# Optimization experiments

Hardware: AMD Instinct MI355X
Metric: run time of the kernel (lower is better)

Reference implementation:

```python
import jax, jax.numpy as jnp
import numpy as np

N = 4096        # nodes
C = 256         # in_channels
E0 = 65536      # edges before adding self-loops
RATIO = 0.5
K = int(np.ceil(RATIO * N))   # pooled nodes (topk)
NEG = 0.2       # leaky relu negative slope


def setup_inputs() -> dict:
    key = jax.random.key(0)
    ks = jax.random.split(key, 12)
    x = jax.random.normal(ks[0], (N, C), jnp.float32)
    src = jax.random.randint(ks[1], (E0,), 0, N)
    off = jax.random.randint(ks[2], (E0,), 1, N)
    dst = (src + off) % N                      # guaranteed no self-loops
    edge_index = jnp.stack([src, dst]).astype(jnp.int32)
    s = 1.0 / np.sqrt(C)
    s2 = 1.0 / np.sqrt(2 * C)
    u = lambda k, shape, b: jax.random.uniform(k, shape, jnp.float32, -b, b)
    return dict(
        x=x, edge_index=edge_index,
        Wq=u(ks[3], (C, C), s), bq=u(ks[4], (C,), s),          # lin_q
        gat_w=u(ks[5], (2 * C,), s2), gat_b=u(ks[6], (1,), s2),  # gat_att
        le1_w=u(ks[7], (C,), s), le1_b=u(ks[8], (1,), s),      # LEConv lin1
        le2_w=u(ks[9], (C,), s),                                # LEConv lin2 (no bias)
        le3_w=u(ks[10], (C,), s), le3_b=u(ks[11], (1,), s),    # LEConv lin3
    )


def _asap(x, edge_index, Wq, bq, gat_w, gat_b, le1_w, le1_b, le2_w, le3_w, le3_b):
    # add_remaining_self_loops (inputs have none -> all N loops, weight 1)
    loops = jnp.arange(N, dtype=edge_index.dtype)
    ei = jnp.concatenate([edge_index, jnp.stack([loops, loops])], axis=1)
    i, j = ei[0], ei[1]          # i: aggregation target, j: neighbor

    x_pool = x                   # GNN is None -> x_pool = x
    xj = x_pool[j]               # [E, C]

    # Master2Token attention: X_q = scatter_max over target i
    Xq = jax.ops.segment_max(xj, i, num_segments=N)       # [N, C]
    Mq = Xq @ Wq + bq                                     # lin_q
    sc = jnp.concatenate([Mq[i], xj], axis=-1) @ gat_w + gat_b[0]  # [E]
    sc = jnp.where(sc > 0, sc, NEG * sc)                  # leaky relu

    # segment softmax over targets i
    m = jax.ops.segment_max(sc, i, num_segments=N)
    e = jnp.exp(sc - m[i])
    z = jax.ops.segment_sum(e, i, num_segments=N)
    score = e / z[i]                                      # dropout_att=0, eval

    # cluster representation
    out = jax.ops.segment_sum(x[j] * score[:, None], i, num_segments=N)  # [N, C]

    # fitness = sigmoid(LEConv(out)): x_i' = lin3(x_i) + sum_j (lin1(x_j) - lin2(x_i))
    a = out @ le1_w + le1_b[0]                            # [N]
    b = out @ le2_w                                       # [N]
    agg = jax.ops.segment_sum(a[j] - b[i], i, num_segments=N)
    fitness = jax.nn.sigmoid(agg + out @ le3_w + le3_b[0])  # [N]

    # topk pooling (single graph -> global top_k)
    fit_k, perm = jax.lax.top_k(fitness, K)
    x_out = out[perm] * fit_k[:, None]                    # [K, C]

    # graph_connectivity: E = S^T A S (dense stand-in for coalesce+spspmm)
    n_idx = jnp.zeros(N, jnp.int32).at[perm].set(jnp.arange(K, dtype=jnp.int32))
    in_perm = jnp.zeros(N, bool).at[perm].set(True)
    sS = jax.lax.stop_gradient(score) * in_perm[i]        # score.detach(), kept-cluster edges
    S = jnp.zeros((N, K), x.dtype).at[j, n_idx[i]].add(sS)   # S[j, new(i)] = score
    A = jnp.zeros((N, N), x.dtype).at[i, j].add(1.0)      # edge_weight None -> ones, coalesced
    Eadj = S.T @ (A @ S)                                  # [K, K]
    # remove_self_loops then add_remaining_self_loops(fill=1)
    Eadj = Eadj - jnp.diag(jnp.diag(Eadj)) + jnp.eye(K, dtype=Eadj.dtype)
    return x_out, Eadj, perm


def reference(x, edge_index, Wq, bq, gat_w, gat_b, le1_w, le1_b, le2_w, le3_w, le3_b):
    return _asap(x, edge_index, Wq, bq, gat_w, gat_b,
                 le1_w, le1_b, le2_w, le3_w, le3_b)
```

## Files before the change

### kernel.cpp

```cpp
#include <hip/hip_runtime.h>
#include <math.h>

constexpr int NN  = 4096;
constexpr int CC  = 256;
constexpr int EE0 = 65536;
constexpr int EE  = 69632;
constexpr int KK  = 2048;
constexpr int SL  = 128;

__device__ __forceinline__ void edge_ij(const int* __restrict__ ei, int e, int& i, int& j) {
    if (e < EE0) { i = ei[e]; j = ei[EE0 + e]; }
    else         { i = e - EE0; j = i; }
}
__device__ __forceinline__ int edge_i(const int* __restrict__ ei, int e) {
    return (e < EE0) ? ei[e] : e - EE0;
}
__device__ __forceinline__ int edge_j(const int* __restrict__ ei, int e) {
    return (e < EE0) ? ei[EE0 + e] : e - EE0;
}

__global__ __launch_bounds__(256) void k_build(const int* __restrict__ ei,
                                               int* cnt_i, int* cnt_j,
                                               int* lst_i, int* lst_j,
                                               const float* __restrict__ Wq, const float* __restrict__ bq,
                                               const float* __restrict__ gat_w, const float* __restrict__ gat_b,
                                               double* wv, double* consts, int EB) {
    if ((int)blockIdx.x < EB) {
        int e = blockIdx.x * 256 + threadIdx.x;
        if (e >= EE) return;
        int i, j; edge_ij(ei, e, i, j);
        int si = atomicAdd(&cnt_i[i], 1);
        lst_i[i * SL + si] = e;
        int sj = atomicAdd(&cnt_j[j], 1);
        lst_j[j * SL + sj] = e;
        return;
    }
    int k = blockIdx.x - EB, c = threadIdx.x, l = c & 63;
    double s = (double)Wq[k * CC + c] * (double)gat_w[c];
    #pragma unroll
    for (int d = 32; d > 0; d >>= 1) s += __shfl_down(s, d, 64);
    __shared__ double red[4];
    if (l == 0) red[c >> 6] = s;
    __syncthreads();
    if (c == 0) wv[k] = red[0] + red[1] + red[2] + red[3];
    if (k == 0 && c == 0) {
        double cb = 0.0;
        for (int q = 0; q < CC; ++q) cb += (double)bq[q] * (double)gat_w[q];
        consts[0] = cb + (double)gat_b[0];
    }
}

__global__ __launch_bounds__(256) void k_attn(const float* __restrict__ x, const int* __restrict__ ei,
                                              const int* __restrict__ cnt_i, const int* __restrict__ lst_i,
                                              const double* __restrict__ wv, const float* __restrict__ gat_w,
                                              const double* __restrict__ consts,
                                              const float* __restrict__ le1_w, const float* __restrict__ le1_b,
                                              const float* __restrict__ le2_w,
                                              const float* __restrict__ le3_w, const float* __restrict__ le3_b,
                                              float* __restrict__ score32, float* __restrict__ out32,
                                              double* a64, double* b64, double* l3v) {
    __shared__ int    sj[SL];
    __shared__ double ssc[SL];
    __shared__ double mz[2];
    __shared__ union { float4 m4[4][64]; double d[4][CC]; } red;

    const int n = blockIdx.x, t = threadIdx.x, g = t >> 6, l = t & 63;
    const int base = n * SL;
    const int deg = cnt_i[n];
    const float* gw2 = gat_w + CC;

    float4 mx = make_float4(-INFINITY, -INFINITY, -INFINITY, -INFINITY);
    for (int p = g; p < deg; p += 4) {
        int e = lst_i[base + p];
        int j = edge_j(ei, e);
        float4 v = ((const float4*)(x + (size_t)j * CC))[l];
        mx.x = fmaxf(mx.x, v.x); mx.y = fmaxf(mx.y, v.y);
        mx.z = fmaxf(mx.z, v.z); mx.w = fmaxf(mx.w, v.w);
        double d = (double)v.x * (double)gw2[4 * l]     + (double)v.y * (double)gw2[4 * l + 1]
                 + (double)v.z * (double)gw2[4 * l + 2] + (double)v.w * (double)gw2[4 * l + 3];
        #pragma unroll
        for (int dd = 32; dd > 0; dd >>= 1) d += __shfl_down(d, dd, 64);
        if (l == 0) { sj[p] = j; ssc[p] = d; }
    }
    red.m4[g][l] = mx;
    __syncthreads();
    if (g == 0) {
        float4 a = red.m4[0][l], b = red.m4[1][l], c2 = red.m4[2][l], d4 = red.m4[3][l];
        float m0 = fmaxf(fmaxf(a.x, b.x), fmaxf(c2.x, d4.x));
        float m1 = fmaxf(fmaxf(a.y, b.y), fmaxf(c2.y, d4.y));
        float m2 = fmaxf(fmaxf(a.z, b.z), fmaxf(c2.z, d4.z));
        float m3 = fmaxf(fmaxf(a.w, b.w), fmaxf(c2.w, d4.w));
        double alph = (double)m0 * wv[4 * l]     + (double)m1 * wv[4 * l + 1]
                    + (double)m2 * wv[4 * l + 2] + (double)m3 * wv[4 * l + 3];
        #pragma unroll
        for (int dd = 32; dd > 0; dd >>= 1) alph += __shfl_down(alph, dd, 64);
        if (l == 0) mz[0] = alph + consts[0];
    }
    __syncthreads();
    double an = mz[0];
    for (int p = t; p < deg; p += 256) {
        double v = an + ssc[p];
        ssc[p] = v > 0.0 ? v : 0.2 * v;
    }
    __syncthreads();
    if (t < 64) {
        double mm = -1e300;
        for (int p = l; p < deg; p += 64) mm = fmax(mm, ssc[p]);
        #pragma unroll
        for (int d = 32; d > 0; d >>= 1) mm = fmax(mm, __shfl_xor(mm, d, 64));
        double z = 0.0;
        for (int p = l; p < deg; p += 64) z += exp(ssc[p] - mm);
        #pragma unroll
        for (int d = 32; d > 0; d >>= 1) z += __shfl_xor(z, d, 64);
        if (l == 0) { mz[0] = mm; mz[1] = 1.0 / z; }
    }
    __syncthreads();
    double mm = mz[0], inv = mz[1];
    for (int p = t; p < deg; p += 256) {
        double sc = exp(ssc[p] - mm) * inv;
        ssc[p] = sc;
        score32[lst_i[base + p]] = (float)sc;
    }
    __syncthreads();
    double a0 = 0, a1 = 0, a2 = 0, a3 = 0;
    for (int p = g; p < deg; p += 4) {
        double sc = ssc[p];
        float4 v = ((const float4*)(x + (size_t)sj[p] * CC))[l];
        a0 += sc * (double)v.x; a1 += sc * (double)v.y;
        a2 += sc * (double)v.z; a3 += sc * (double)v.w;
    }
    red.d[g][4 * l + 0] = a0; red.d[g][4 * l + 1] = a1;
    red.d[g][4 * l + 2] = a2; red.d[g][4 * l + 3] = a3;
    __syncthreads();
    if (g == 0) {
        double o0 = red.d[0][4*l]   + red.d[1][4*l]   + red.d[2][4*l]   + red.d[3][4*l];
        double o1 = red.d[0][4*l+1] + red.d[1][4*l+1] + red.d[2][4*l+1] + red.d[3][4*l+1];
        double o2 = red.d[0][4*l+2] + red.d[1][4*l+2] + red.d[2][4*l+2] + red.d[3][4*l+2];
        double o3 = red.d[0][4*l+3] + red.d[1][4*l+3] + red.d[2][4*l+3] + red.d[3][4*l+3];
        float4 ov; ov.x = (float)o0; ov.y = (float)o1; ov.z = (float)o2; ov.w = (float)o3;
        ((float4*)(out32 + (size_t)n * CC))[l] = ov;
        float4 w1 = ((const float4*)le1_w)[l];
        float4 w2 = ((const float4*)le2_w)[l];
        float4 w3 = ((const float4*)le3_w)[l];
        double s1 = o0 * (double)w1.x + o1 * (double)w1.y + o2 * (double)w1.z + o3 * (double)w1.w;
        double s2 = o0 * (double)w2.x + o1 * (double)w2.y + o2 * (double)w2.z + o3 * (double)w2.w;
        double s3 = o0 * (double)w3.x + o1 * (double)w3.y + o2 * (double)w3.z + o3 * (double)w3.w;
        #pragma unroll
        for (int dd = 32; dd > 0; dd >>= 1) {
            s1 += __shfl_down(s1, dd, 64);
            s2 += __shfl_down(s2, dd, 64);
            s3 += __shfl_down(s3, dd, 64);
        }
        if (l == 0) {
            a64[n] = s1 + (double)le1_b[0];
            b64[n] = s2;
            l3v[n] = s3 + (double)le3_b[0];
        }
    }
}

__global__ __launch_bounds__(256) void k_zlog(const int* __restrict__ ei,
                                              const int* __restrict__ cnt_i, const int* __restrict__ lst_i,
                                              const double* __restrict__ a64, const double* __restrict__ b64,
                                              const double* __restrict__ l3v, double* zlog) {
    int n = blockIdx.x * 4 + (threadIdx.x >> 6);
    int l = threadIdx.x & 63;
    int deg = cnt_i[n];
    int base = n * SL;
    double acc = 0.0;
    for (int p = l; p < deg; p += 64) {
        int e = lst_i[base + p];
        acc += a64[edge_j(ei, e)];
    }
    #pragma unroll
    for (int d = 32; d > 0; d >>= 1) acc += __shfl_xor(acc, d, 64);
    if (l == 0) zlog[n] = acc - (double)deg * b64[n] + l3v[n];
}

__global__ __launch_bounds__(256) void k_rank(const double* __restrict__ zlog,
                                              const float* __restrict__ out32,
                                              int* __restrict__ perm, int* __restrict__ n_idx,
                                              float* __restrict__ xout, float* __restrict__ operm) {
    int n = blockIdx.x, t = threadIdx.x;
    double zn = zlog[n];
    int cnt = 0;
    #pragma unroll
    for (int u = 0; u < NN / 256; ++u) {
        int m = t + u * 256;
        double zm = zlog[m];
        cnt += ((zm > zn) || (zm == zn && m < n)) ? 1 : 0;
    }
    #pragma unroll
    for (int d = 32; d > 0; d >>= 1) cnt += __shfl_down(cnt, d, 64);
    __shared__ int red[4];
    __shared__ int rr;
    if ((t & 63) == 0) red[t >> 6] = cnt;
    __syncthreads();
    if (t == 0) {
        int r = red[0] + red[1] + red[2] + red[3];
        rr = r;
        if (r < KK) {
            perm[r] = n;
            n_idx[n] = r;
            operm[r] = (float)n;
        } else {
            n_idx[n] = -1;
        }
    }
    __syncthreads();
    int r = rr;
    if (r < KK) {
        double fit = 1.0 / (1.0 + exp(-zn));
        xout[(size_t)r * CC + t] = (float)((double)out32[(size_t)n * CC + t] * fit);
    }
}

__global__ __launch_bounds__(256) void k_colval(const int* __restrict__ ei,
                                                const int* __restrict__ cnt_j, const int* __restrict__ lst_j,
                                                const int* __restrict__ n_idx, const float* __restrict__ score32,
                                                int* __restrict__ colj, float* __restrict__ svalj) {
    int p = blockIdx.x * 256 + threadIdx.x;
    int n = p >> 7, s = p & (SL - 1);
    if (s >= cnt_j[n]) return;
    int e = lst_j[p];
    colj[p] = n_idx[edge_i(ei, e)];
    svalj[p] = score32[e];
}

__global__ __launch_bounds__(256) void k_eadj(const int* __restrict__ ei,
                                              const int* __restrict__ cnt_i, const int* __restrict__ lst_i,
                                              const int* __restrict__ cnt_j,
                                              const int* __restrict__ perm,
                                              const float* __restrict__ score32,
                                              const int* __restrict__ colj, const float* __restrict__ svalj,
                                              float* __restrict__ Ead) {
    __shared__ float row[KK];
    int r = blockIdx.x, t = threadIdx.x;
    float4 z4 = make_float4(0.f, 0.f, 0.f, 0.f);
    for (int c = t; c < KK / 4; c += 256) ((float4*)row)[c] = z4;
    __syncthreads();
    int n = perm[r];
    int deg = cnt_i[n];
    int base = n * SL;
    int grp = t >> 5, lane = t & 31;
    for (int p = grp; p < deg; p += 8) {
        int e = lst_i[base + p];
        float s1 = score32[e];
        int j = edge_j(ei, e);
        int cj = cnt_j[j], jb = j * SL;
        for (int q = lane; q < cj; q += 32) {
            int c = colj[jb + q];
            if (c >= 0) atomicAdd(&row[c], s1 * svalj[jb + q]);
        }
    }
    __syncthreads();
    float* __restrict__ erow = Ead + (size_t)r * KK;
    for (int c4 = t; c4 < KK / 4; c4 += 256) {
        float4 v = ((float4*)row)[c4];
        int base4 = c4 * 4;
        int dr = r - base4;
        if (dr >= 0 && dr < 4) ((float*)&v)[dr] = 1.0f;
        ((float4*)erow)[c4] = v;
    }
}

extern "C" void kernel_launch(void* const* d_in, const int* in_sizes, int n_in,
                              void* d_out, int out_size, void* d_ws, size_t ws_size,
                              hipStream_t stream) {
    const float* x     = (const float*)d_in[0];
    const int*   ei    = (const int*)d_in[1];
    const float* Wq    = (const float*)d_in[2];
    const float* bq    = (const float*)d_in[3];
    const float* gat_w = (const float*)d_in[4];
    const float* gat_b = (const float*)d_in[5];
    const float* le1_w = (const float*)d_in[6];
    const float* le1_b = (const float*)d_in[7];
    const float* le2_w = (const float*)d_in[8];
    const float* le3_w = (const float*)d_in[9];
    const float* le3_b = (const float*)d_in[10];

    float* xout  = (float*)d_out;
    float* Ead   = xout + (size_t)KK * CC;
    float* operm = Ead + (size_t)KK * KK;

    char* w = (char*)d_ws;
    auto alloc = [&](size_t bytes) -> void* {
        void* p = (void*)w;
        w += (bytes + 255) & ~(size_t)255;
        return p;
    };
    float*  score32= (float*)alloc(EE * 4);
    float*  out32  = (float*)alloc((size_t)NN * CC * 4);
    double* a64    = (double*)alloc(NN * 8);
    double* b64    = (double*)alloc(NN * 8);
    double* l3v    = (double*)alloc(NN * 8);
    double* zlog   = (double*)alloc(NN * 8);
    double* wv     = (double*)alloc(CC * 8);
    double* consts = (double*)alloc(64);
    int* cnt_i = (int*)alloc(NN * 4);
    int* cnt_j = (int*)alloc(NN * 4);
    int* lst_i = (int*)alloc((size_t)NN * SL * 4);
    int* lst_j = (int*)alloc((size_t)NN * SL * 4);
    int* n_idx = (int*)alloc(NN * 4);
    int* perm  = (int*)alloc(KK * 4);
    int*   colj  = (int*)alloc((size_t)NN * SL * 4);
    float* svalj = (float*)alloc((size_t)NN * SL * 4);

    hipMemsetAsync(cnt_i, 0, 2 * NN * 4, stream);

    const int EB = (EE + 255) / 256;

    k_build<<<EB + CC, 256, 0, stream>>>(ei, cnt_i, cnt_j, lst_i, lst_j,
                                         Wq, bq, gat_w, gat_b, wv, consts, EB);
    k_attn<<<NN, 256, 0, stream>>>(x, ei, cnt_i, lst_i, wv, gat_w, consts,
                                   le1_w, le1_b, le2_w, le3_w, le3_b,
                                   score32, out32, a64, b64, l3v);
    k_zlog<<<NN / 4, 256, 0, stream>>>(ei, cnt_i, lst_i, a64, b64, l3v, zlog);
    k_rank<<<NN, 256, 0, stream>>>(zlog, out32, perm, n_idx, xout, operm);
    k_colval<<<NN * SL / 256, 256, 0, stream>>>(ei, cnt_j, lst_j, n_idx, score32, colj, svalj);
    k_eadj<<<KK, 256, 0, stream>>>(ei, cnt_i, lst_i, cnt_j, perm, score32, colj, svalj, Ead);
}
```

Before: 152.8 us.

## Precompute per-node GAT scores, fuse zlog into attention, drop colval pass

Computes the neighbor half of the GAT score once per node in k_build instead of once per edge inside k_attn. Folds the k_zlog gather into k_attn as atomic scatter-adds over outgoing edges, with zlog zeroed by the existing memset. Removes k_colval so k_eadj looks up column index and score on the fly through lst_j and n_idx. This cuts two kernel launches and redundant per-edge dot products, at the cost of double-precision atomics and extra indirect loads in the hot eadj loop. Atomic ordering makes zlog, and therefore the top-k ranking, non-deterministic.

```diff
diff --git a/kernel.cpp b/kernel.cpp
--- a/kernel.cpp
+++ b/kernel.cpp
@@ -22,11 +22,13 @@
 __global__ __launch_bounds__(256) void k_build(const int* __restrict__ ei,
                                                int* cnt_i, int* cnt_j,
                                                int* lst_i, int* lst_j,
+                                               const float* __restrict__ x,
                                                const float* __restrict__ Wq, const float* __restrict__ bq,
                                                const float* __restrict__ gat_w, const float* __restrict__ gat_b,
-                                               double* wv, double* consts, int EB) {
+                                               double* wv, double* consts, double* beta_node, int EB) {
+    const int t = threadIdx.x, g = t >> 6, l = t & 63;
     if ((int)blockIdx.x < EB) {
-        int e = blockIdx.x * 256 + threadIdx.x;
+        int e = blockIdx.x * 256 + t;
         if (e >= EE) return;
         int i, j; edge_ij(ei, e, i, j);
         int si = atomicAdd(&cnt_i[i], 1);
@@ -35,52 +37,65 @@
         lst_j[j * SL + sj] = e;
         return;
     }
-    int k = blockIdx.x - EB, c = threadIdx.x, l = c & 63;
-    double s = (double)Wq[k * CC + c] * (double)gat_w[c];
+    if ((int)blockIdx.x < EB + CC) {
+        int k = blockIdx.x - EB;
+        double s = (double)Wq[k * CC + t] * (double)gat_w[t];
+        #pragma unroll
+        for (int d = 32; d > 0; d >>= 1) s += __shfl_down(s, d, 64);
+        __shared__ double red[4];
+        if (l == 0) red[g] = s;
+        __syncthreads();
+        if (t == 0) wv[k] = red[0] + red[1] + red[2] + red[3];
+        if (k == 0 && t == 0) {
+            double cb = 0.0;
+            for (int q = 0; q < CC; ++q) cb += (double)bq[q] * (double)gat_w[q];
+            consts[0] = cb + (double)gat_b[0];
+        }
+        return;
+    }
+    int m = (blockIdx.x - EB - CC) * 4 + g;
+    const float* gw2 = gat_w + CC;
+    float4 v = ((const float4*)(x + (size_t)m * CC))[l];
+    double s = (double)v.x * (double)gw2[4 * l]     + (double)v.y * (double)gw2[4 * l + 1]
+             + (double)v.z * (double)gw2[4 * l + 2] + (double)v.w * (double)gw2[4 * l + 3];
     #pragma unroll
     for (int d = 32; d > 0; d >>= 1) s += __shfl_down(s, d, 64);
-    __shared__ double red[4];
-    if (l == 0) red[c >> 6] = s;
-    __syncthreads();
-    if (c == 0) wv[k] = red[0] + red[1] + red[2] + red[3];
-    if (k == 0 && c == 0) {
-        double cb = 0.0;
-        for (int q = 0; q < CC; ++q) cb += (double)bq[q] * (double)gat_w[q];
-        consts[0] = cb + (double)gat_b[0];
-    }
+    if (l == 0) beta_node[m] = s;
 }
 
 __global__ __launch_bounds__(256) void k_attn(const float* __restrict__ x, const int* __restrict__ ei,
                                               const int* __restrict__ cnt_i, const int* __restrict__ lst_i,
-                                              const double* __restrict__ wv, const float* __restrict__ gat_w,
+                                              const int* __restrict__ cnt_j, const int* __restrict__ lst_j,
+                                              const double* __restrict__ wv, const double* __restrict__ beta_node,
                                               const double* __restrict__ consts,
                                               const float* __restrict__ le1_w, const float* __restrict__ le1_b,
                                               const float* __restrict__ le2_w,
                                               const float* __restrict__ le3_w, const float* __restrict__ le3_b,
                                               float* __restrict__ score32, float* __restrict__ out32,
-                                              double* a64, double* b64, double* l3v) {
+                                              double* __restrict__ zlog) {
     __shared__ int    sj[SL];
     __shared__ double ssc[SL];
     __shared__ double mz[2];
+    __shared__ double bcast;
     __shared__ union { float4 m4[4][64]; double d[4][CC]; } red;
 
     const int n = blockIdx.x, t = threadIdx.x, g = t >> 6, l = t & 63;
     const int base = n * SL;
     const int deg = cnt_i[n];
-    const float* gw2 = gat_w + CC;
+
+    for (int p = t; p < deg; p += 256) {
+        int e = lst_i[base + p];
+        int j = edge_j(ei, e);
+        sj[p] = j;
+        ssc[p] = beta_node[j];
+    }
+    __syncthreads();
 
     float4 mx = make_float4(-INFINITY, -INFINITY, -INFINITY, -INFINITY);
     for (int p = g; p < deg; p += 4) {
-        int e = lst_i[base + p];
-        int j = edge_j(ei, e);
-        float4 v = ((const float4*)(x + (size_t)j * CC))[l];
+        float4 v = ((const float4*)(x + (size_t)sj[p] * CC))[l];
         mx.x = fmaxf(mx.x, v.x); mx.y = fmaxf(mx.y, v.y);
         mx.z = fmaxf(mx.z, v.z); mx.w = fmaxf(mx.w, v.w);
-        double d = (double)v.x * (double)gw2[4 * l]     + (double)v.y * (double)gw2[4 * l + 1]
-                 + (double)v.z * (double)gw2[4 * l + 2] + (double)v.w * (double)gw2[4 * l + 3];
-        #pragma unroll
-        for (int dd = 32; dd > 0; dd >>= 1) d += __shfl_down(d, dd, 64);
-        if (l == 0) { sj[p] = j; ssc[p] = d; }
     }
     red.m4[g][l] = mx;
     __syncthreads();
@@ -152,29 +167,20 @@
             s3 += __shfl_down(s3, dd, 64);
         }
         if (l == 0) {
-            a64[n] = s1 + (double)le1_b[0];
-            b64[n] = s2;
-            l3v[n] = s3 + (double)le3_b[0];
-        }
-    }
-}
-
-__global__ __launch_bounds__(256) void k_zlog(const int* __restrict__ ei,
-                                              const int* __restrict__ cnt_i, const int* __restrict__ lst_i,
-                                              const double* __restrict__ a64, const double* __restrict__ b64,
-                                              const double* __restrict__ l3v, double* zlog) {
-    int n = blockIdx.x * 4 + (threadIdx.x >> 6);
-    int l = threadIdx.x & 63;
-    int deg = cnt_i[n];
-    int base = n * SL;
-    double acc = 0.0;
-    for (int p = l; p < deg; p += 64) {
-        int e = lst_i[base + p];
-        acc += a64[edge_j(ei, e)];
-    }
-    #pragma unroll
-    for (int d = 32; d > 0; d >>= 1) acc += __shfl_xor(acc, d, 64);
-    if (l == 0) zlog[n] = acc - (double)deg * b64[n] + l3v[n];
+            double a64n = s1 + (double)le1_b[0];
+            double b64n = s2;
+            double l3vn = s3 + (double)le3_b[0];
+            atomicAdd(&zlog[n], l3vn - (double)deg * b64n);
+            bcast = a64n;
+        }
+    }
+    __syncthreads();
+    double a64n = bcast;
+    int cj = cnt_j[n], jb = n * SL;
+    for (int p = t; p < cj; p += 256) {
+        int e = lst_j[jb + p];
+        atomicAdd(&zlog[edge_i(ei, e)], a64n);
+    }
 }
 
 __global__ __launch_bounds__(256) void k_rank(const double* __restrict__ zlog,
@@ -215,24 +221,12 @@
     }
 }
 
-__global__ __launch_bounds__(256) void k_colval(const int* __restrict__ ei,
-                                                const int* __restrict__ cnt_j, const int* __restrict__ lst_j,
-                                                const int* __restrict__ n_idx, const float* __restrict__ score32,
-                                                int* __restrict__ colj, float* __restrict__ svalj) {
-    int p = blockIdx.x * 256 + threadIdx.x;
-    int n = p >> 7, s = p & (SL - 1);
-    if (s >= cnt_j[n]) return;
-    int e = lst_j[p];
-    colj[p] = n_idx[edge_i(ei, e)];
-    svalj[p] = score32[e];
-}
-
 __global__ __launch_bounds__(256) void k_eadj(const int* __restrict__ ei,
                                               const int* __restrict__ cnt_i, const int* __restrict__ lst_i,
-                                              const int* __restrict__ cnt_j,
+                                              const int* __restrict__ cnt_j, const int* __restrict__ lst_j,
+                                              const int* __restrict__ n_idx,
                                               const int* __restrict__ perm,
                                               const float* __restrict__ score32,
-                                              const int* __restrict__ colj, const float* __restrict__ svalj,
                                               float* __restrict__ Ead) {
     __shared__ float row[KK];
     int r = blockIdx.x, t = threadIdx.x;
@@ -249,8 +243,9 @@
         int j = edge_j(ei, e);
         int cj = cnt_j[j], jb = j * SL;
         for (int q = lane; q < cj; q += 32) {
-            int c = colj[jb + q];
-            if (c >= 0) atomicAdd(&row[c], s1 * svalj[jb + q]);
+            int e2 = lst_j[jb + q];
+            int c = n_idx[edge_i(ei, e2)];
+            if (c >= 0) atomicAdd(&row[c], s1 * score32[e2]);
         }
     }
     __syncthreads();
@@ -289,34 +284,28 @@
         w += (bytes + 255) & ~(size_t)255;
         return p;
     };
+    int*    cnt_i  = (int*)alloc(NN * 4);
+    int*    cnt_j  = (int*)alloc(NN * 4);
+    double* zlog   = (double*)alloc(NN * 8);
     float*  score32= (float*)alloc(EE * 4);
     float*  out32  = (float*)alloc((size_t)NN * CC * 4);
-    double* a64    = (double*)alloc(NN * 8);
-    double* b64    = (double*)alloc(NN * 8);
-    double* l3v    = (double*)alloc(NN * 8);
-    double* zlog   = (double*)alloc(NN * 8);
+    double* beta_node = (double*)alloc(NN * 8);
     double* wv     = (double*)alloc(CC * 8);
     double* consts = (double*)alloc(64);
-    int* cnt_i = (int*)alloc(NN * 4);
-    int* cnt_j = (int*)alloc(NN * 4);
     int* lst_i = (int*)alloc((size_t)NN * SL * 4);
     int* lst_j = (int*)alloc((size_t)NN * SL * 4);
     int* n_idx = (int*)alloc(NN * 4);
     int* perm  = (int*)alloc(KK * 4);
-    int*   colj  = (int*)alloc((size_t)NN * SL * 4);
-    float* svalj = (float*)alloc((size_t)NN * SL * 4);
-
-    hipMemsetAsync(cnt_i, 0, 2 * NN * 4, stream);
+
+    hipMemsetAsync(cnt_i, 0, 2 * NN * 4 + NN * 8, stream);
 
     const int EB = (EE + 255) / 256;
 
-    k_build<<<EB + CC, 256, 0, stream>>>(ei, cnt_i, cnt_j, lst_i, lst_j,
-                                         Wq, bq, gat_w, gat_b, wv, consts, EB);
-    k_attn<<<NN, 256, 0, stream>>>(x, ei, cnt_i, lst_i, wv, gat_w, consts,
+    k_build<<<EB + CC + NN / 4, 256, 0, stream>>>(ei, cnt_i, cnt_j, lst_i, lst_j, x,
+                                                  Wq, bq, gat_w, gat_b, wv, consts, beta_node, EB);
+    k_attn<<<NN, 256, 0, stream>>>(x, ei, cnt_i, lst_i, cnt_j, lst_j, wv, beta_node, consts,
                                    le1_w, le1_b, le2_w, le3_w, le3_b,
-                                   score32, out32, a64, b64, l3v);
-    k_zlog<<<NN / 4, 256, 0, stream>>>(ei, cnt_i, lst_i, a64, b64, l3v, zlog);
+                                   score32, out32, zlog);
     k_rank<<<NN, 256, 0, stream>>>(zlog, out32, perm, n_idx, xout, operm);
-    k_colval<<<NN * SL / 256, 256, 0, stream>>>(ei, cnt_j, lst_j, n_idx, score32, colj, svalj);
-    k_eadj<<<KK, 256, 0, stream>>>(ei, cnt_i, lst_i, cnt_j, perm, score32, colj, svalj, Ead);
-}
+    k_eadj<<<KK, 256, 0, stream>>>(ei, cnt_i, lst_i, cnt_j, lst_j, n_idx, perm, score32, Ead);
+}
```

New measurement: 155.4 us. About the same (+1.7%).
